# Kernel optimization log

Hardware: AMD Instinct MI355X
Metric: run time of the kernel (lower is better)

Reference implementation:

```python
import jax, jax.numpy as jnp
import numpy as np

N = 4096  # number of rows == cols (init arg N)
D = 64    # point feature dimension


def setup_inputs() -> dict:
    key = jax.random.key(0)
    kx, ky = jax.random.split(key)
    return {
        "xINP": jax.random.normal(kx, (N, D), dtype=jnp.float32),
        "yINP": jax.random.normal(ky, (N, D), dtype=jnp.float32),
    }


def _pairwise_euclidean(x, y):
    # scipy.spatial.distance_matrix default p=2: sqrt(sum((xi - yj)^2))
    sq = (jnp.sum(x * x, axis=1)[:, None]
          + jnp.sum(y * y, axis=1)[None, :]
          - 2.0 * (x @ y.T))
    return jnp.sqrt(jnp.maximum(sq, 0.0))  # [N, N]


def _greedy_match(cost):
    # Greedy bipartite matching: visit all (i, j) pairs in ascending cost
    # order; accept a pair iff both row i and col j are still unmatched.
    n, m = cost.shape
    order = jnp.argsort(cost.reshape(-1))          # stable sort, like python sorted
    rows = (order // m).astype(jnp.int32)          # [n*m]
    cols = (order % m).astype(jnp.int32)           # [n*m]

    def step(carry, ij):
        rm, cm = carry
        i, j = ij
        free = (rm[i] == -1) & (cm[j] == -1)
        rm = rm.at[i].set(jnp.where(free, j, rm[i]))
        cm = cm.at[j].set(jnp.where(free, i, cm[j]))
        return (rm, cm), None

    init = (jnp.full((n,), -1, dtype=jnp.int32),   # row_to_col_match_vec
            jnp.full((m,), -1, dtype=jnp.int32))   # col_to_row_match_vec
    (_, cm), _ = jax.lax.scan(step, init, (rows, cols))
    return cm


def reference(xINP, yINP):
    cost = _pairwise_euclidean(xINP, yINP)   # [N, N]
    return _greedy_match(cost)               # [N] int32: col_to_row_match_vec
```

## Files before the change

### kernel.cpp

```cpp
#include <hip/hip_runtime.h>
#include <stdint.h>

#define NN 4096
#define DD 64
#define GCOL 16
#define CCH 16
#define RCHK 8
#define TMAX 112
#define TGMAX 512
#define NROUNDS 17
#define ROUNDS_FB 32

typedef unsigned long long u64;
typedef unsigned int u32;

#define RESC 0xFFFFFFFFFFFFFFFEull
#define EMPTY (~0ull)

__device__ __forceinline__ u64 pk(float d, u32 idx) {
  return (((u64)__float_as_uint(d)) << 32) | (u64)idx;
}

__device__ __forceinline__ float distfly(const float* __restrict__ x,
                                         const float* __restrict__ y,
                                         float xxi, float yyj, int i, int j) {
  const float* xi = x + (size_t)i * DD;
  const float* yj = y + (size_t)j * DD;
  float dot = 0.f;
#pragma unroll
  for (int k = 0; k < DD; ++k) dot = fmaf(xi[k], yj[k], dot);
  float sq = (xxi + yyj) - 2.0f * dot;
  return sqrtf(fmaxf(sq, 0.f));
}

__global__ void k_init(const float* __restrict__ x, const float* __restrict__ y,
                       float* xx, float* yy, int* rm, int* cm, int* FR, int* Fcnt,
                       u64* rowbest, u64* rowpart, u64* colpart) {
  int i = blockIdx.x * blockDim.x + threadIdx.x;
  if (i < NN) {
    const float* xi = x + (size_t)i * DD;
    const float* yi = y + (size_t)i * DD;
    float sx = 0.f, sy = 0.f;
#pragma unroll
    for (int k = 0; k < DD; ++k) { sx = fmaf(xi[k], xi[k], sx); sy = fmaf(yi[k], yi[k], sy); }
    xx[i] = sx; yy[i] = sy;
    rm[i] = -1; cm[i] = -1; FR[i] = i;
    rowbest[i] = EMPTY;
#pragma unroll
    for (int h = 0; h < RCHK; ++h) rowpart[(size_t)h * NN + i] = RESC;
#pragma unroll
    for (int g = 0; g < CCH; ++g) colpart[(size_t)g * NN + i] = RESC;
    if (i == 0) *Fcnt = NN;
  }
}

__global__ void k_build(const float* __restrict__ x, const float* __restrict__ y,
                        const float* __restrict__ xx, const float* __restrict__ yy,
                        float* __restrict__ C) {
  __shared__ float xs[64][65];
  __shared__ float ys[64][65];
  int t = threadIdx.x;
  int bi = blockIdx.y * 64, bj = blockIdx.x * 64;
  for (int e = t; e < 64 * 64; e += 256) {
    int r = e >> 6, c = e & 63;
    xs[r][c] = x[(size_t)(bi + r) * DD + c];
    ys[r][c] = y[(size_t)(bj + r) * DD + c];
  }
  __syncthreads();
  int tx = t & 15, ty = t >> 4;
  float acc[4][4];
#pragma unroll
  for (int r = 0; r < 4; ++r)
#pragma unroll
    for (int c = 0; c < 4; ++c) acc[r][c] = 0.f;
#pragma unroll
  for (int k = 0; k < 64; ++k) {
    float a[4], b[4];
#pragma unroll
    for (int r = 0; r < 4; ++r) a[r] = xs[ty * 4 + r][k];
#pragma unroll
    for (int c = 0; c < 4; ++c) b[c] = ys[tx * 4 + c][k];
#pragma unroll
    for (int r = 0; r < 4; ++r)
#pragma unroll
      for (int c = 0; c < 4; ++c) acc[r][c] = fmaf(a[r], b[c], acc[r][c]);
  }
#pragma unroll
  for (int r = 0; r < 4; ++r) {
    int i = bi + ty * 4 + r;
    float xxi = xx[i];
    float4 v;
    float* vp = (float*)&v;
#pragma unroll
    for (int c = 0; c < 4; ++c) {
      int j = bj + tx * 4 + c;
      float sq = (xxi + yy[j]) - 2.0f * acc[r][c];
      vp[c] = sqrtf(fmaxf(sq, 0.f));
    }
    *(float4*)(C + (size_t)i * NN + bj + tx * 4) = v;
  }
}

__global__ void k_round2(const float* __restrict__ C, const int* __restrict__ rm,
                         const int* __restrict__ cm, u64* __restrict__ rowbest,
                         u64* __restrict__ rowpart, u64* __restrict__ colpart) {
  __shared__ u64 wbest[4];
  __shared__ u64 part[4][64];
  int b = blockIdx.x;
  int t = threadIdx.x;
  int lane = t & 63, w = t >> 6;
  if (b < NN) {
    int i = b;
    if (rm[i] != -1) return;
    u64 rb = rowbest[i];
    u32 jb = (u32)rb;
    if (jb < NN && cm[jb] == -1) return;
    const float* Ci = C + (size_t)i * NN;
    u64 mycv = EMPTY;
#pragma unroll
    for (int pass = 0; pass < 2; ++pass) {
      int h = w + pass * 4;
      u64 e = rowpart[(size_t)h * NN + i];
      u32 je = (u32)e;
      bool stale = (e != EMPTY) && !(je < NN && cm[je] == -1);
      u64 cv = e;
      if (stale) {
        int j0 = h * 512 + lane * 8;
        float4 v0 = *(const float4*)(Ci + j0);
        float4 v1 = *(const float4*)(Ci + j0 + 4);
        int4 m0 = *(const int4*)(cm + j0);
        int4 m1 = *(const int4*)(cm + j0 + 4);
        const float* vp0 = (const float*)&v0; const int* mp0 = (const int*)&m0;
        const float* vp1 = (const float*)&v1; const int* mp1 = (const int*)&m1;
        u64 bl = EMPTY;
#pragma unroll
        for (int c = 0; c < 4; ++c)
          if (mp0[c] == -1) { u64 k2 = pk(vp0[c], (u32)(j0 + c)); if (k2 < bl) bl = k2; }
#pragma unroll
        for (int c = 0; c < 4; ++c)
          if (mp1[c] == -1) { u64 k2 = pk(vp1[c], (u32)(j0 + 4 + c)); if (k2 < bl) bl = k2; }
#pragma unroll
        for (int md = 1; md < 64; md <<= 1) {
          u64 o = __shfl_xor(bl, md, 64);
          if (o < bl) bl = o;
        }
        cv = bl;
        if (lane == 0) rowpart[(size_t)h * NN + i] = bl;
      }
      if (cv < mycv) mycv = cv;
    }
    if (lane == 0) wbest[w] = mycv;
    __syncthreads();
    if (t == 0) {
      u64 best = wbest[0];
#pragma unroll
      for (int w2 = 1; w2 < 4; ++w2) if (wbest[w2] < best) best = wbest[w2];
      rowbest[i] = best;
    }
  } else {
    int idx = b - NN;
    int cb = idx & 63, g = idx >> 6;
    int j = cb * 64 + lane;
    u64* slot = colpart + (size_t)g * NN + j;
    bool stale_c = false;
    if (cm[j] == -1) {
      u64 e = *slot;
      if (e != EMPTY) { u32 io = (u32)e; stale_c = !(io < NN && rm[io] == -1); }
    }
    u64 best = EMPTY;
    if (stale_c) {
      int i0 = g * 256 + w * 64;
      for (int i = i0; i < i0 + 64; ++i) {
        if (rm[i] != -1) continue;
        u64 key = pk(C[(size_t)i * NN + j], (u32)i);
        if (key < best) best = key;
      }
    }
    part[w][lane] = best;
    __syncthreads();
    if (w == 0 && stale_c) {
      u64 b0 = part[0][lane];
#pragma unroll
      for (int q = 1; q < 4; ++q) if (part[q][lane] < b0) b0 = part[q][lane];
      *slot = b0;
    }
  }
}

__global__ void k_accept3(const u64* __restrict__ colpart, const u64* __restrict__ rowbest,
                          int* rm, int* cm, int* Fcnt) {
  if (*Fcnt == 0) return;
  int j = blockIdx.x * 256 + threadIdx.x;
  if (cm[j] != -1) return;
  u64 best = EMPTY;
#pragma unroll
  for (int g = 0; g < CCH; ++g) {
    u64 v = colpart[(size_t)g * NN + j];
    if (v < best) best = v;
  }
  u32 io = (u32)best;
  if (io >= NN) return;
  int i = (int)io;
  if (rm[i] == -1 && (u32)(rowbest[i] & 0xffffffffu) == (u32)j) {
    rm[i] = j; cm[j] = i;
    atomicSub(Fcnt, 1);
  }
}

__global__ __launch_bounds__(256) void k_endgame(const float* __restrict__ C,
                                                 int* rm, int* cm, int* FRg,
                                                 float* __restrict__ G) {
  __shared__ __align__(16) char shb[54272];
  int* sFR5 = (int*)shb;
  int* sFC5 = (int*)(shb + 2048);
  float* Csub = (float*)(shb + 4096);
  u64* rkey2 = (u64*)(shb + 4096);
  int* rcol2 = (int*)(shb + 8192);
  int* cfree2 = (int*)(shb + 10240);
  int* dl = (int*)(shb + 12288);
  __shared__ int sF, sG, sc_star, scnt;
  __shared__ u64 rkey[TMAX];
  __shared__ int rcol[TMAX];
  __shared__ int cfree[TMAX];
  __shared__ u64 wred[4];
  __shared__ u64 red[256];
  __shared__ int redi[256];
  int t = threadIdx.x;
  if (t == 0) { sF = 0; sG = 0; }
  __syncthreads();
  for (int i = t; i < NN; i += 256)
    if (rm[i] == -1) { int p = atomicAdd(&sF, 1); if (p < TGMAX) sFR5[p] = i; }
  for (int j = t; j < NN; j += 256)
    if (cm[j] == -1) { int p = atomicAdd(&sG, 1); if (p < TGMAX) sFC5[p] = j; }
  __syncthreads();
  int F = sF;
  if (F == 0) return;
  if (F <= TMAX) {
    for (int r = (t >> 6); r < F; r += 4) {
      const float* Ci = C + (size_t)sFR5[r] * NN;
      for (int c = (t & 63); c < F; c += 64) Csub[r * F + c] = Ci[sFC5[c]];
    }
    for (int c = t; c < F; c += 256) cfree[c] = 1;
    __syncthreads();
    for (int r = t; r < F; r += 256) {
      const float* row = Csub + r * F;
      u64 bk = ~0ull; int bc = 0; int ig = sFR5[r];
      for (int c = 0; c < F; ++c) {
        u64 k = (((u64)__float_as_uint(row[c])) << 24) | (u32)(ig * NN + sFC5[c]);
        if (k < bk) { bk = k; bc = c; }
      }
      rkey[r] = bk; rcol[r] = bc;
    }
    __syncthreads();
    for (int it = 0; it < F; ++it) {
      u64 kb = ~0ull;
      if (t < F && rkey[t] != ~0ull) kb = (rkey[t] << 8) | (u64)(u32)t;
      for (int s = 32; s > 0; s >>= 1) {
        u64 o = __shfl_down(kb, s, 64);
        if (o < kb) kb = o;
      }
      if ((t & 63) == 0) wred[t >> 6] = kb;
      __syncthreads();
      if (t == 0) {
        u64 bmin = wred[0];
#pragma unroll
        for (int wv = 1; wv < 4; ++wv) if (wred[wv] < bmin) bmin = wred[wv];
        int rstar = (int)(bmin & 255);
        if (rstar >= F) rstar = 0;
        int cstar = rcol[rstar];
        sc_star = cstar;
        int i = sFR5[rstar], j = sFC5[cstar];
        rm[i] = j; cm[j] = i;
        rkey[rstar] = ~0ull; cfree[cstar] = 0;
      }
      __syncthreads();
      int cs = sc_star;
      for (int r = t; r < F; r += 256) {
        if (rkey[r] != ~0ull && rcol[r] == cs) {
          const float* row = Csub + r * F;
          u64 bk = ~0ull; int bc = 0; int ig = sFR5[r];
          for (int c = 0; c < F; ++c) {
            if (!cfree[c]) continue;
            u64 k = (((u64)__float_as_uint(row[c])) << 24) | (u32)(ig * NN + sFC5[c]);
            if (k < bk) { bk = k; bc = c; }
          }
          rkey[r] = bk; rcol[r] = bc;
        }
      }
      __syncthreads();
    }
  } else if (F <= TGMAX && G != nullptr) {
    for (int r = (t >> 6); r < F; r += 4) {
      const float* Ci = C + (size_t)sFR5[r] * NN;
      for (int c = (t & 63); c < F; c += 64) G[(size_t)r * F + c] = Ci[sFC5[c]];
    }
    for (int c = t; c < F; c += 256) cfree2[c] = 1;
    __syncthreads();
    for (int r = t; r < F; r += 256) {
      const float* row = G + (size_t)r * F;
      u64 bk = ~0ull; int bc = 0; int ig = sFR5[r];
      for (int c = 0; c < F; ++c) {
        u64 k = (((u64)__float_as_uint(row[c])) << 24) | (u32)(ig * NN + sFC5[c]);
        if (k < bk) { bk = k; bc = c; }
      }
      rkey2[r] = bk; rcol2[r] = bc;
    }
    __syncthreads();
    for (int it = 0; it < F; ++it) {
      u64 lv = ~0ull; int la = 0;
      for (int r = t; r < F; r += 256)
        if (rkey2[r] < lv) { lv = rkey2[r]; la = r; }
      red[t] = lv; redi[t] = la;
      __syncthreads();
      for (int s = 128; s > 0; s >>= 1) {
        if (t < s && red[t + s] < red[t]) { red[t] = red[t + s]; redi[t] = redi[t + s]; }
        __syncthreads();
      }
      if (t == 0) {
        int rstar = redi[0];
        int cstar = rcol2[rstar];
        sc_star = cstar;
        rm[sFR5[rstar]] = sFC5[cstar]; cm[sFC5[cstar]] = sFR5[rstar];
        rkey2[rstar] = ~0ull; cfree2[cstar] = 0;
        scnt = 0;
      }
      __syncthreads();
      int cs = sc_star;
      for (int r = t; r < F; r += 256)
        if (rkey2[r] != ~0ull && rcol2[r] == cs) { int p = atomicAdd(&scnt, 1); dl[p] = r; }
      __syncthreads();
      int nd = scnt;
      for (int d = 0; d < nd; ++d) {
        int r = dl[d];
        const float* Gr = G + (size_t)r * F;
        int ig = sFR5[r];
        u64 lb = ~0ull; int lc = 0;
        for (int c = t; c < F; c += 256) {
          if (!cfree2[c]) continue;
          u64 k = (((u64)__float_as_uint(Gr[c])) << 24) | (u32)(ig * NN + sFC5[c]);
          if (k < lb) { lb = k; lc = c; }
        }
        red[t] = lb; redi[t] = lc;
        __syncthreads();
        for (int s = 128; s > 0; s >>= 1) {
          if (t < s && red[t + s] < red[t]) { red[t] = red[t + s]; redi[t] = redi[t + s]; }
          __syncthreads();
        }
        if (t == 0) { rkey2[r] = red[0]; rcol2[r] = redi[0]; }
        __syncthreads();
      }
    }
  } else {
    for (int it = 0; it < NN; ++it) {
      if (t == 0) scnt = 0;
      __syncthreads();
      for (int i = t; i < NN; i += 256)
        if (rm[i] == -1) { int p = atomicAdd(&scnt, 1); FRg[p] = i; }
      __syncthreads();
      int Fa = scnt;
      if (Fa == 0) break;
      u64 best = ~0ull;
      int total = Fa * NN;
      for (int idx = t; idx < total; idx += 256) {
        int bb2 = idx >> 12, j = idx & 4095;
        if (cm[j] != -1) continue;
        int i = FRg[bb2];
        u64 key = pk(C[(size_t)i * NN + j], (u32)(i * NN + j));
        if (key < best) best = key;
      }
      red[t] = best;
      __syncthreads();
      for (int s = 128; s > 0; s >>= 1) {
        if (t < s) { if (red[t + s] < red[t]) red[t] = red[t + s]; }
        __syncthreads();
      }
      if (t == 0) {
        u32 lo = (u32)red[0];
        rm[lo >> 12] = lo & 4095; cm[lo & 4095] = lo >> 12;
      }
      __syncthreads();
    }
  }
}

template <bool USEC>
__global__ void k_rowpass(const float* __restrict__ C,
                          const float* __restrict__ x, const float* __restrict__ y,
                          const float* __restrict__ xx, const float* __restrict__ yy,
                          const int* __restrict__ cm, const int* __restrict__ FR,
                          const int* __restrict__ Fcnt, u64* __restrict__ rowbest) {
  int b = blockIdx.x;
  if (b >= *Fcnt) return;
  int i = FR[b];
  __shared__ float xsh[DD];
  __shared__ u64 red[256];
  int t = threadIdx.x;
  if (!USEC) { if (t < DD) xsh[t] = x[(size_t)i * DD + t]; }
  __syncthreads();
  float xxi = xx[i];
  u64 best = ~0ull;
  for (int j = t; j < NN; j += 256) {
    if (cm[j] != -1) continue;
    float d;
    if (USEC) {
      d = C[(size_t)i * NN + j];
    } else {
      const float* yj = y + (size_t)j * DD;
      float dot = 0.f;
#pragma unroll
      for (int k = 0; k < DD; ++k) dot = fmaf(xsh[k], yj[k], dot);
      float sq = (xxi + yy[j]) - 2.0f * dot;
      d = sqrtf(fmaxf(sq, 0.f));
    }
    u64 key = pk(d, (u32)j);
    if (key < best) best = key;
  }
  red[t] = best;
  __syncthreads();
  for (int s = 128; s > 0; s >>= 1) {
    if (t < s) { if (red[t + s] < red[t]) red[t] = red[t + s]; }
    __syncthreads();
  }
  if (t == 0) rowbest[i] = red[0];
}

template <bool USEC>
__global__ void k_colpass(const float* __restrict__ C,
                          const float* __restrict__ x, const float* __restrict__ y,
                          const float* __restrict__ xx, const float* __restrict__ yy,
                          const int* __restrict__ cm, const int* __restrict__ FR,
                          const int* __restrict__ Fcnt, u64* __restrict__ colpart) {
  int t = threadIdx.x;
  int j = blockIdx.x * 256 + t;
  int g = blockIdx.y;
  int F = *Fcnt;
  if (F == 0) return;
  int b0 = (g * F) / GCOL, b1 = ((g + 1) * F) / GCOL;
  u64 best = ~0ull;
  if (cm[j] == -1) {
    float yyj = yy[j];
    if (USEC) {
      for (int b = b0; b < b1; ++b) {
        int i = FR[b];
        u64 key = pk(C[(size_t)i * NN + j], (u32)i);
        if (key < best) best = key;
      }
    } else {
      float4 yr[16];
      const float4* yj4 = (const float4*)(y + (size_t)j * DD);
#pragma unroll
      for (int q = 0; q < 16; ++q) yr[q] = yj4[q];
      for (int b = b0; b < b1; ++b) {
        int i = FR[b];
        const float4* xi4 = (const float4*)(x + (size_t)i * DD);
        float dot = 0.f;
#pragma unroll
        for (int q = 0; q < 16; ++q) {
          float4 a = xi4[q], bb = yr[q];
          dot = fmaf(a.x, bb.x, dot); dot = fmaf(a.y, bb.y, dot);
          dot = fmaf(a.z, bb.z, dot); dot = fmaf(a.w, bb.w, dot);
        }
        float sq = (xx[i] + yyj) - 2.0f * dot;
        float d = sqrtf(fmaxf(sq, 0.f));
        u64 key = pk(d, (u32)i);
        if (key < best) best = key;
      }
    }
  }
  colpart[(size_t)g * NN + j] = best;
}

__global__ void k_accept(const u64* __restrict__ colpart, const u64* __restrict__ rowbest,
                         int* rm, int* cm, int* FR, int* Fcnt) {
  __shared__ int scnt;
  int t = threadIdx.x;
  if (*Fcnt == 0) return;
  for (int j = t; j < NN; j += 1024) {
    if (cm[j] != -1) continue;
    u64 best = ~0ull;
#pragma unroll
    for (int g = 0; g < GCOL; ++g) {
      u64 v = colpart[(size_t)g * NN + j];
      if (v < best) best = v;
    }
    u32 io = (u32)best;
    if (io >= NN) continue;
    int i = (int)io;
    if (rm[i] == -1 && (u32)(rowbest[i] & 0xffffffffu) == (u32)j) { rm[i] = j; cm[j] = i; }
  }
  __syncthreads();
  if (t == 0) scnt = 0;
  __syncthreads();
  for (int i = t; i < NN; i += 1024)
    if (rm[i] == -1) { int p = atomicAdd(&scnt, 1); FR[p] = i; }
  __syncthreads();
  if (t == 0) *Fcnt = scnt;
}

template <bool USEC>
__global__ void k_cleanup(const float* __restrict__ C,
                          const float* __restrict__ x, const float* __restrict__ y,
                          const float* __restrict__ xx, const float* __restrict__ yy,
                          int* rm, int* cm, int* FR) {
  __shared__ int scnt;
  __shared__ u64 red[1024];
  int t = threadIdx.x;
  for (int it = 0; it < NN; ++it) {
    if (t == 0) scnt = 0;
    __syncthreads();
    for (int i = t; i < NN; i += 1024)
      if (rm[i] == -1) { int p = atomicAdd(&scnt, 1); FR[p] = i; }
    __syncthreads();
    int F = scnt;
    if (F == 0) break;
    u64 best = ~0ull;
    int total = F * NN;
    for (int idx = t; idx < total; idx += 1024) {
      int b = idx >> 12;
      int j = idx & 4095;
      if (cm[j] != -1) continue;
      int i = FR[b];
      float d;
      if (USEC) d = C[(size_t)i * NN + j];
      else d = distfly(x, y, xx[i], yy[j], i, j);
      u64 key = pk(d, (u32)(i * NN + j));
      if (key < best) best = key;
    }
    red[t] = best;
    __syncthreads();
    for (int s = 512; s > 0; s >>= 1) {
      if (t < s) { if (red[t + s] < red[t]) red[t] = red[t + s]; }
      __syncthreads();
    }
    if (t == 0) {
      u32 lo = (u32)red[0];
      int i = lo >> 12, j = lo & 4095;
      rm[i] = j; cm[j] = i;
    }
    __syncthreads();
  }
}

extern "C" void kernel_launch(void* const* d_in, const int* in_sizes, int n_in,
                              void* d_out, int out_size, void* d_ws, size_t ws_size,
                              hipStream_t stream) {
  const float* x = (const float*)d_in[0];
  const float* y = (const float*)d_in[1];
  int* cm = (int*)d_out;

  char* w = (char*)d_ws;
  float* xx = (float*)(w + 0);
  float* yy = (float*)(w + 16384);
  int* rm = (int*)(w + 32768);
  int* FR = (int*)(w + 49152);
  int* Fcnt = (int*)(w + 65536);
  u64* rowbest = (u64*)(w + 65664);
  u64* rowpart = (u64*)(w + 98432);
  u64* colpart = (u64*)(w + 360704);
  float* C = (float*)(w + 1048576);
  float* G = (float*)(w + 68157440);

  size_t need_c = 1048576 + (size_t)NN * NN * 4;
  size_t need_g = 68157440 + (size_t)TGMAX * TGMAX * 4;
  bool usec = ws_size >= need_c;
  bool useg = ws_size >= need_g;

  k_init<<<dim3(16), 256, 0, stream>>>(x, y, xx, yy, rm, cm, FR, Fcnt,
                                       rowbest, rowpart, colpart);
  if (usec) {
    k_build<<<dim3(64, 64), 256, 0, stream>>>(x, y, xx, yy, C);
    for (int r = 0; r < NROUNDS; ++r) {
      k_round2<<<dim3(NN + 64 * CCH), 256, 0, stream>>>(C, rm, cm, rowbest, rowpart, colpart);
      k_accept3<<<dim3(16), 256, 0, stream>>>(colpart, rowbest, rm, cm, Fcnt);
    }
    k_endgame<<<dim3(1), 256, 0, stream>>>(C, rm, cm, FR, useg ? G : nullptr);
  } else {
    for (int r = 0; r < ROUNDS_FB; ++r) {
      k_rowpass<false><<<dim3(NN), 256, 0, stream>>>(nullptr, x, y, xx, yy, cm, FR, Fcnt, rowbest);
      k_colpass<false><<<dim3(16, GCOL), 256, 0, stream>>>(nullptr, x, y, xx, yy, cm, FR, Fcnt, colpart);
      k_accept<<<dim3(1), 1024, 0, stream>>>(colpart, rowbest, rm, cm, FR, Fcnt);
    }
    k_cleanup<false><<<dim3(1), 1024, 0, stream>>>(nullptr, x, y, xx, yy, rm, cm, FR);
  }
}
```

Baseline: 731.3 us.

## Replace serial endgame with mutual-best parallel matching rounds and fewer global rounds

The single-block endgame, which accepted one pair per iteration through block reductions, becomes a loop of parallel rounds. Each round accepts every free pair whose row-best and column-best point at each other, then recomputes stale row and column bests. The endgame size limit grows to 1024 and the global round loop drops from 17 to 12 launches, moving more of the work into the endgame. This trades serial reduction and sync cost for per-thread O(F) rescans over G in global memory. Column scans read G with stride F, which may be slow for large F.

```diff
diff --git a/kernel.cpp b/kernel.cpp
--- a/kernel.cpp
+++ b/kernel.cpp
@@ -6,13 +6,13 @@
 #define GCOL 16
 #define CCH 16
 #define RCHK 8
-#define TMAX 112
-#define TGMAX 512
-#define NROUNDS 17
+#define TGMAX 1024
+#define NROUNDS 12
 #define ROUNDS_FB 32
 
 typedef unsigned long long u64;
 typedef unsigned int u32;
+typedef unsigned short u16;
 
 #define RESC 0xFFFFFFFFFFFFFFFEull
 #define EMPTY (~0ull)
@@ -207,148 +207,88 @@
   }
 }
 
-__global__ __launch_bounds__(256) void k_endgame(const float* __restrict__ C,
-                                                 int* rm, int* cm, int* FRg,
-                                                 float* __restrict__ G) {
-  __shared__ __align__(16) char shb[54272];
-  int* sFR5 = (int*)shb;
-  int* sFC5 = (int*)(shb + 2048);
-  float* Csub = (float*)(shb + 4096);
-  u64* rkey2 = (u64*)(shb + 4096);
-  int* rcol2 = (int*)(shb + 8192);
-  int* cfree2 = (int*)(shb + 10240);
-  int* dl = (int*)(shb + 12288);
-  __shared__ int sF, sG, sc_star, scnt;
-  __shared__ u64 rkey[TMAX];
-  __shared__ int rcol[TMAX];
-  __shared__ int cfree[TMAX];
-  __shared__ u64 wred[4];
+__global__ __launch_bounds__(256) void k_endgame2(const float* __restrict__ C,
+                                                  int* rm, int* cm, int* FRg,
+                                                  float* __restrict__ G) {
+  __shared__ u16 sFR[TGMAX], sFC[TGMAX], rcol[TGMAX], crow[TGMAX];
+  __shared__ unsigned char rfree[TGMAX], cfree[TGMAX];
+  __shared__ u64 rkey[TGMAX];
+  __shared__ int sF, sG2, nmat, scnt;
   __shared__ u64 red[256];
-  __shared__ int redi[256];
-  int t = threadIdx.x;
-  if (t == 0) { sF = 0; sG = 0; }
+  int t = threadIdx.x;
+  if (t == 0) { sF = 0; sG2 = 0; nmat = 0; }
   __syncthreads();
   for (int i = t; i < NN; i += 256)
-    if (rm[i] == -1) { int p = atomicAdd(&sF, 1); if (p < TGMAX) sFR5[p] = i; }
+    if (rm[i] == -1) { int p = atomicAdd(&sF, 1); if (p < TGMAX) sFR[p] = (u16)i; }
   for (int j = t; j < NN; j += 256)
-    if (cm[j] == -1) { int p = atomicAdd(&sG, 1); if (p < TGMAX) sFC5[p] = j; }
+    if (cm[j] == -1) { int p = atomicAdd(&sG2, 1); if (p < TGMAX) sFC[p] = (u16)j; }
   __syncthreads();
   int F = sF;
   if (F == 0) return;
-  if (F <= TMAX) {
-    for (int r = (t >> 6); r < F; r += 4) {
-      const float* Ci = C + (size_t)sFR5[r] * NN;
-      for (int c = (t & 63); c < F; c += 64) Csub[r * F + c] = Ci[sFC5[c]];
-    }
-    for (int c = t; c < F; c += 256) cfree[c] = 1;
+  if (F <= TGMAX && G != nullptr) {
+    for (int r = t >> 6; r < F; r += 4) {
+      const float* Ci = C + (size_t)sFR[r] * NN;
+      for (int c = t & 63; c < F; c += 64) G[(size_t)r * F + c] = Ci[sFC[c]];
+    }
+    for (int v = t; v < F; v += 256) { rfree[v] = 1; cfree[v] = 1; }
     __syncthreads();
     for (int r = t; r < F; r += 256) {
-      const float* row = Csub + r * F;
-      u64 bk = ~0ull; int bc = 0; int ig = sFR5[r];
+      const float* Mr = G + (size_t)r * F;
+      u64 bk = ~0ull; int bc = 0;
+      u32 base = (u32)sFR[r] * NN;
       for (int c = 0; c < F; ++c) {
-        u64 k = (((u64)__float_as_uint(row[c])) << 24) | (u32)(ig * NN + sFC5[c]);
+        u64 k = (((u64)__float_as_uint(Mr[c])) << 24) | (u64)(base + sFC[c]);
         if (k < bk) { bk = k; bc = c; }
       }
-      rkey[r] = bk; rcol[r] = bc;
-    }
-    __syncthreads();
-    for (int it = 0; it < F; ++it) {
-      u64 kb = ~0ull;
-      if (t < F && rkey[t] != ~0ull) kb = (rkey[t] << 8) | (u64)(u32)t;
-      for (int s = 32; s > 0; s >>= 1) {
-        u64 o = __shfl_down(kb, s, 64);
-        if (o < kb) kb = o;
-      }
-      if ((t & 63) == 0) wred[t >> 6] = kb;
-      __syncthreads();
-      if (t == 0) {
-        u64 bmin = wred[0];
-#pragma unroll
-        for (int wv = 1; wv < 4; ++wv) if (wred[wv] < bmin) bmin = wred[wv];
-        int rstar = (int)(bmin & 255);
-        if (rstar >= F) rstar = 0;
-        int cstar = rcol[rstar];
-        sc_star = cstar;
-        int i = sFR5[rstar], j = sFC5[cstar];
-        rm[i] = j; cm[j] = i;
-        rkey[rstar] = ~0ull; cfree[cstar] = 0;
-      }
-      __syncthreads();
-      int cs = sc_star;
+      rkey[r] = bk; rcol[r] = (u16)bc;
+    }
+    for (int c = t; c < F; c += 256) {
+      u64 bk = ~0ull; int br = 0;
+      for (int r = 0; r < F; ++r) {
+        u64 k = (((u64)__float_as_uint(G[(size_t)r * F + c])) << 24)
+                | (u64)((u32)sFR[r] * NN + sFC[c]);
+        if (k < bk) { bk = k; br = r; }
+      }
+      crow[c] = (u16)br;
+    }
+    __syncthreads();
+    for (int round = 0; round < F + 1; ++round) {
+      for (int c = t; c < F; c += 256) {
+        if (!cfree[c]) continue;
+        int r = crow[c];
+        if (rfree[r] && rcol[r] == c) {
+          rm[sFR[r]] = sFC[c];
+          cm[sFC[c]] = sFR[r];
+          rfree[r] = 0; cfree[c] = 0;
+          atomicAdd(&nmat, 1);
+        }
+      }
+      __syncthreads();
+      if (nmat >= F) break;
       for (int r = t; r < F; r += 256) {
-        if (rkey[r] != ~0ull && rcol[r] == cs) {
-          const float* row = Csub + r * F;
-          u64 bk = ~0ull; int bc = 0; int ig = sFR5[r];
-          for (int c = 0; c < F; ++c) {
-            if (!cfree[c]) continue;
-            u64 k = (((u64)__float_as_uint(row[c])) << 24) | (u32)(ig * NN + sFC5[c]);
-            if (k < bk) { bk = k; bc = c; }
-          }
-          rkey[r] = bk; rcol[r] = bc;
+        if (!rfree[r] || cfree[rcol[r]]) continue;
+        const float* Mr = G + (size_t)r * F;
+        u64 bk = ~0ull; int bc = 0;
+        u32 base = (u32)sFR[r] * NN;
+        for (int c = 0; c < F; ++c) {
+          if (!cfree[c]) continue;
+          u64 k = (((u64)__float_as_uint(Mr[c])) << 24) | (u64)(base + sFC[c]);
+          if (k < bk) { bk = k; bc = c; }
         }
-      }
-      __syncthreads();
-    }
-  } else if (F <= TGMAX && G != nullptr) {
-    for (int r = (t >> 6); r < F; r += 4) {
-      const float* Ci = C + (size_t)sFR5[r] * NN;
-      for (int c = (t & 63); c < F; c += 64) G[(size_t)r * F + c] = Ci[sFC5[c]];
-    }
-    for (int c = t; c < F; c += 256) cfree2[c] = 1;
-    __syncthreads();
-    for (int r = t; r < F; r += 256) {
-      const float* row = G + (size_t)r * F;
-      u64 bk = ~0ull; int bc = 0; int ig = sFR5[r];
-      for (int c = 0; c < F; ++c) {
-        u64 k = (((u64)__float_as_uint(row[c])) << 24) | (u32)(ig * NN + sFC5[c]);
-        if (k < bk) { bk = k; bc = c; }
-      }
-      rkey2[r] = bk; rcol2[r] = bc;
-    }
-    __syncthreads();
-    for (int it = 0; it < F; ++it) {
-      u64 lv = ~0ull; int la = 0;
-      for (int r = t; r < F; r += 256)
-        if (rkey2[r] < lv) { lv = rkey2[r]; la = r; }
-      red[t] = lv; redi[t] = la;
-      __syncthreads();
-      for (int s = 128; s > 0; s >>= 1) {
-        if (t < s && red[t + s] < red[t]) { red[t] = red[t + s]; redi[t] = redi[t + s]; }
-        __syncthreads();
-      }
-      if (t == 0) {
-        int rstar = redi[0];
-        int cstar = rcol2[rstar];
-        sc_star = cstar;
-        rm[sFR5[rstar]] = sFC5[cstar]; cm[sFC5[cstar]] = sFR5[rstar];
-        rkey2[rstar] = ~0ull; cfree2[cstar] = 0;
-        scnt = 0;
-      }
-      __syncthreads();
-      int cs = sc_star;
-      for (int r = t; r < F; r += 256)
-        if (rkey2[r] != ~0ull && rcol2[r] == cs) { int p = atomicAdd(&scnt, 1); dl[p] = r; }
-      __syncthreads();
-      int nd = scnt;
-      for (int d = 0; d < nd; ++d) {
-        int r = dl[d];
-        const float* Gr = G + (size_t)r * F;
-        int ig = sFR5[r];
-        u64 lb = ~0ull; int lc = 0;
-        for (int c = t; c < F; c += 256) {
-          if (!cfree2[c]) continue;
-          u64 k = (((u64)__float_as_uint(Gr[c])) << 24) | (u32)(ig * NN + sFC5[c]);
-          if (k < lb) { lb = k; lc = c; }
+        rkey[r] = bk; rcol[r] = (u16)bc;
+      }
+      for (int c = t; c < F; c += 256) {
+        if (!cfree[c] || rfree[crow[c]]) continue;
+        u64 bk = ~0ull; int br = 0;
+        for (int r = 0; r < F; ++r) {
+          if (!rfree[r]) continue;
+          u64 k = (((u64)__float_as_uint(G[(size_t)r * F + c])) << 24)
+                  | (u64)((u32)sFR[r] * NN + sFC[c]);
+          if (k < bk) { bk = k; br = r; }
         }
-        red[t] = lb; redi[t] = lc;
-        __syncthreads();
-        for (int s = 128; s > 0; s >>= 1) {
-          if (t < s && red[t + s] < red[t]) { red[t] = red[t + s]; redi[t] = redi[t + s]; }
-          __syncthreads();
-        }
-        if (t == 0) { rkey2[r] = red[0]; rcol2[r] = redi[0]; }
-        __syncthreads();
-      }
+        crow[c] = (u16)br;
+      }
+      __syncthreads();
     }
   } else {
     for (int it = 0; it < NN; ++it) {
@@ -569,11 +509,12 @@
                                        rowbest, rowpart, colpart);
   if (usec) {
     k_build<<<dim3(64, 64), 256, 0, stream>>>(x, y, xx, yy, C);
-    for (int r = 0; r < NROUNDS; ++r) {
+    int nr = useg ? NROUNDS : 20;
+    for (int r = 0; r < nr; ++r) {
       k_round2<<<dim3(NN + 64 * CCH), 256, 0, stream>>>(C, rm, cm, rowbest, rowpart, colpart);
       k_accept3<<<dim3(16), 256, 0, stream>>>(colpart, rowbest, rm, cm, Fcnt);
     }
-    k_endgame<<<dim3(1), 256, 0, stream>>>(C, rm, cm, FR, useg ? G : nullptr);
+    k_endgame2<<<dim3(1), 256, 0, stream>>>(C, rm, cm, FR, useg ? G : nullptr);
   } else {
     for (int r = 0; r < ROUNDS_FB; ++r) {
       k_rowpass<false><<<dim3(NN), 256, 0, stream>>>(nullptr, x, y, xx, yy, cm, FR, Fcnt, rowbest);
```

After: 1.208 ms. +65.2%, slower.
